# Kernel optimization log

Measured on AMD Instinct MI355X. Metric: run time of the kernel, lower is better.

Reference implementation:

```python
import jax, jax.numpy as jnp
import numpy as np

C_LOGIT = 10.0  # logit clipping constant C from __init__
NEG_INF = -1e8


def setup_inputs() -> dict:
    key = jax.random.key(0)
    ks = jax.random.split(key, 10)
    B, S, E, H = 512, 256, 128, 128
    u = lambda k, sh: jax.random.uniform(k, sh, jnp.float32, -0.1, 0.1)
    return {
        "low_context_vector": jax.random.normal(ks[0], (B, S, E), jnp.float32),
        "original_node": jax.random.uniform(ks[1], (S, 2), jnp.float32),
        "mask": jnp.zeros((B, S), jnp.float32),
        # learned parameters
        "low_init_w": jax.random.uniform(ks[2], (2 * E,), jnp.float32, -1.0, 1.0),
        "Wc": u(ks[3], (E, E)),   "bc": u(ks[4], (E,)),     # low_h_context_embed
        "Wv": u(ks[5], (2 * E, E)), "bv": u(ks[6], (E,)),   # low_v_weight_embed
        "Wq": u(ks[7], (E, H)),                              # pointer query proj
        "Wref": u(ks[8], (E, H)),                            # pointer ref proj
        "v": u(ks[9], (H,)),                                 # pointer score vector
    }


def _decode(cv, mask, low_init_w, Wc, bc, Wv, bv, Wq, Wref, v, key):
    B, S, E = cv.shape
    h_bar = jnp.mean(cv, axis=1) @ Wc + bc              # [B,E]
    rest0 = low_init_w @ Wv + bv                        # [E]
    query0 = h_bar + rest0[None, :]                     # [B,E]
    ref = cv @ Wref                                     # [B,S,H], hoisted out of loop
    mask = mask.at[:, 0].set(1.0)                       # start node visited
    keys = jax.random.split(key, S - 1)
    binds = jnp.arange(B)

    def step(carry, k):
        mask, query, init_h, i = carry
        u_ = jnp.tanh((query @ Wq)[:, None, :] + ref) @ v      # [B,S]
        logits = jnp.where(mask > 0, NEG_INF, C_LOGIT * jnp.tanh(u_))
        logp = jax.nn.log_softmax(logits, axis=-1)
        g = jax.random.gumbel(k, logits.shape, logits.dtype)
        idx = jnp.argmax(logits + g, axis=-1)                  # Categorical sample, [B]
        lp = jnp.take_along_axis(logp, idx[:, None], axis=1)[:, 0]
        mask = mask.at[binds, idx].set(1.0)
        h = cv[binds, idx]                                     # gathered embedding [B,E]
        init_h = jnp.where(i == 0, h, init_h)                  # first pick cached
        query = h_bar + (jnp.concatenate([init_h, h], axis=-1) @ Wv + bv)
        return (mask, query, init_h, i + 1), (idx, lp)

    init = (mask, query0, jnp.zeros((B, E), cv.dtype), jnp.int32(0))
    _, (idxs, lps) = jax.lax.scan(step, init, keys)
    return idxs.T, lps.T  # [B, S-1] each


def reference(low_context_vector, original_node, mask, low_init_w, Wc, bc, Wv, bv, Wq, Wref, v):
    # original_node only feeds a printed local_reward in the torch code; it does
    # not affect the returned (indices, log_probs), so it is unused here.
    return _decode(low_context_vector, mask, low_init_w, Wc, bc, Wv, bv, Wq, Wref, v,
                   jax.random.key(42))
```

## Files before the change

### kernel.cpp

```cpp
#include <hip/hip_runtime.h>
#include <hip/hip_bf16.h>
#include <stdint.h>
#include <math.h>

#define NBATCH 512
#define NS 256
#define NE 128
#define NH 128
#define NSTEPS 255
#define NEGINF -1e8f
#define SENT_NEG -1e30f

__device__ __forceinline__ uint32_t rotl32(uint32_t x, uint32_t r) {
  return (x << r) | (x >> (32u - r));
}

__device__ __forceinline__ void tf2x32(uint32_t k0, uint32_t k1,
                                       uint32_t x0, uint32_t x1,
                                       uint32_t& o0, uint32_t& o1) {
  uint32_t ks2 = k0 ^ k1 ^ 0x1BD11BDAu;
  x0 += k0; x1 += k1;
#define TF_R4(a,b,c,d) \
  x0 += x1; x1 = rotl32(x1,a); x1 ^= x0; \
  x0 += x1; x1 = rotl32(x1,b); x1 ^= x0; \
  x0 += x1; x1 = rotl32(x1,c); x1 ^= x0; \
  x0 += x1; x1 = rotl32(x1,d); x1 ^= x0;
  TF_R4(13,15,26,6)   x0 += k1;  x1 += ks2 + 1u;
  TF_R4(17,29,16,24)  x0 += ks2; x1 += k0 + 2u;
  TF_R4(13,15,26,6)   x0 += k0;  x1 += k1 + 3u;
  TF_R4(17,29,16,24)  x0 += k1;  x1 += ks2 + 4u;
  TF_R4(13,15,26,6)   x0 += ks2; x1 += k0 + 5u;
#undef TF_R4
  o0 = x0; o1 = x1;
}

__device__ __forceinline__ float gumbel_of(uint2 key, uint32_t j) {
  uint32_t o0, o1;
  tf2x32(key.x, key.y, 0u, j, o0, o1);
  uint32_t bits = o0 ^ o1;
  float f = __uint_as_float((bits >> 9) | 0x3f800000u) - 1.0f;
  float u = (f == 0.0f) ? 1.17549435e-38f : f;
  float l1 = -logf(u);
  return -logf(l1);
}

__device__ __forceinline__ float nr_tanh(float x) {
  const float Chi = 2.8853900432586670f;
  const float Clo = 3.8519259822379735e-08f;
  float m = fmaf(x, Chi, x * Clo);
  m = fminf(m, 126.0f);
  float tt = __builtin_amdgcn_exp2f(m);
  float d  = tt + 1.0f;
  float r  = __builtin_amdgcn_rcpf(d);
  r = r * fmaf(-d, r, 2.0f);
  return fmaf(-2.0f, r, 1.0f);
}

__device__ __forceinline__ double dot32(const float4* __restrict__ a,
                                        const float4* __restrict__ bp) {
  double s = 0.0;
#pragma unroll
  for (int q = 0; q < 8; ++q) {
    float4 x = a[q], y = bp[q];
    s += (double)x.x * (double)y.x + (double)x.y * (double)y.y
       + (double)x.z * (double)y.z + (double)x.w * (double)y.w;
  }
  return s;
}

__device__ __forceinline__ double dot4d(float4 a, float4 b) {
  return ((double)a.x * (double)b.x + (double)a.y * (double)b.y)
       + ((double)a.z * (double)b.z + (double)a.w * (double)b.w);
}

__global__ void k1_mats(const float* __restrict__ Wv, const float* __restrict__ Wq,
                        const float* __restrict__ liw, const float* __restrict__ bvv,
                        float* __restrict__ M1T, float* __restrict__ M2T,
                        float* __restrict__ rest0) {
  int e = blockIdx.x, h = threadIdx.x;
  __shared__ float wrow[NE];
  if (e < 256) {
    wrow[h] = Wv[e * NE + h];
    __syncthreads();
    double a = 0.0;
    for (int k = 0; k < NE; ++k) a += (double)wrow[k] * (double)Wq[k * NH + h];
    if (e < 128) M1T[h * NE + e] = (float)a;
    else         M2T[h * NE + (e - 128)] = (float)a;
  } else {
    double a = 0.0;
    for (int k = 0; k < 2 * NE; ++k) a += (double)liw[k] * (double)Wv[k * NE + h];
    rest0[h] = (float)a + bvv[h];
  }
}

__global__ void k2_base(const float* __restrict__ cv, const float* __restrict__ Wc,
                        const float* __restrict__ bc, const float* __restrict__ bvv,
                        const float* __restrict__ Wq, const float* __restrict__ rest0,
                        double* __restrict__ qqbase, float* __restrict__ qq0) {
  int b = blockIdx.x, h = threadIdx.x;
  int b256 = b << 8;
  __shared__ float meanL[NE], hbarL[NE];
  double ms = 0.0;
  for (int s = 0; s < NS; ++s) ms += (double)cv[((size_t)b256 + s) * NE + h];
  meanL[h] = (float)(ms * (1.0 / 256.0));
  __syncthreads();
  double a = 0.0;
  for (int e = 0; e < NE; ++e) a += (double)meanL[e] * (double)Wc[e * NE + h];
  hbarL[h] = (float)a + bc[h];
  __syncthreads();
  double ab = 0.0, a0 = 0.0;
  for (int k = 0; k < NE; ++k) {
    double w = (double)Wq[k * NH + h];
    ab += (double)(hbarL[k] + bvv[k]) * w;
    a0 += (double)(hbarL[k] + rest0[k]) * w;
  }
  qqbase[(size_t)b * NH + h] = ab;
  qq0[(size_t)b * NH + h] = (float)a0;
}

__global__ __launch_bounds__(256)
void k_a2v2(const float* __restrict__ cv, const float* __restrict__ M2T,
            double* __restrict__ A2) {
  const int b  = blockIdx.x >> 3;
  const int s0 = (blockIdx.x & 7) << 5;
  const int t  = threadIdx.x;
  const int sl = t >> 7;
  const int h  = t & 127;
  const int b256 = b << 8;
  __shared__ float cvS[32][129];
  for (int idx = t; idx < 32 * NE; idx += 256) {
    int r = idx >> 7, c = idx & 127;
    cvS[r][c] = cv[((size_t)(b256 + s0 + r)) * NE + c];
  }
  __syncthreads();
  float4 m2r[32];
  {
    const float4* m2p = (const float4*)(M2T + (size_t)h * NE);
#pragma unroll
    for (int q = 0; q < 32; ++q) m2r[q] = m2p[q];
  }
#pragma unroll 1
  for (int it = 0; it < 16; ++it) {
    const int sLoc = (it << 1) + sl;
    const float4* cr4 = (const float4*)&cvS[sLoc][0];
    double c0 = 0, c1 = 0, c2 = 0, c3 = 0;
#pragma unroll
    for (int q = 0; q < 8; ++q) {
      c0 += dot4d(cr4[q * 4 + 0], m2r[q * 4 + 0]);
      c1 += dot4d(cr4[q * 4 + 1], m2r[q * 4 + 1]);
      c2 += dot4d(cr4[q * 4 + 2], m2r[q * 4 + 2]);
      c3 += dot4d(cr4[q * 4 + 3], m2r[q * 4 + 3]);
    }
    A2[((size_t)(b256 + s0 + sLoc)) * NH + h] = (c0 + c1) + (c2 + c3);
  }
}

struct MainSh {
  alignas(16) float  qq[NH];
  alignas(16) float  vvf[NH];
  alignas(8)  double partA[NS];
  float  logitArr[NS];
  alignas(8)  double base128[NH];
  uint2  keyL[NSTEPS];
  float  redV[8];
  float  redS[8];
  int    redI[8];
};

struct PreSh {
  float cvS[NS][33];
  float wS[32][NH];
};

template <int MODE>
__global__ __launch_bounds__(512, 4)
void decode_main(const float* __restrict__ cv,
                 const float* __restrict__ mask_in,
                 const float* __restrict__ Wref,
                 const float* __restrict__ vvec,
                 const double* __restrict__ qqbase,
                 const float* __restrict__ M1T,
                 const float* __restrict__ M2T,
                 const float* __restrict__ qq0,
                 const double* __restrict__ A2,
                 float* __restrict__ out) {
  const int b = blockIdx.x;
  const int t = threadIdx.x;
  const int b256 = b << 8;
  const int i = t & 255;
  const int halfo = t >> 8;
  const int hb = halfo << 6;

  __shared__ union { PreSh pre; MainSh m; } sh;
  __shared__ short rowIdA[NS], rowIdB[NS], posA[NS], posB[NS];
  __shared__ int nActSh[2], jSh[2], tmp8[4];
  __shared__ alignas(16) float refScratch[NE];

  bool act0 = false;
  if (t < NS) {
    act0 = !((t == 0) || (mask_in[(size_t)b256 + t] > 0.0f));
    uint64_t mb = __ballot(act0);
    int lane = t & 63, w = t >> 6;
    int pre = __popcll(mb & (((uint64_t)1 << lane) - 1));
    if (lane == 0) tmp8[w] = (int)__popcll(mb);
    posA[t] = (short)pre;
  }
  __syncthreads();
  if (t < NS) {
    int base = 0;
    for (int k = 0; k < (t >> 6); ++k) base += tmp8[k];
    int p = base + (int)posA[t];
    if (act0) rowIdA[p] = (short)t;
    posA[t] = (short)p;
  }
  if (t == 0) {
    nActSh[0] = tmp8[0] + tmp8[1] + tmp8[2] + tmp8[3];
    jSh[0] = -1;
  }
  __syncthreads();
  const int nAct0 = nActSh[0];

  const int myRow0 = (i < nAct0) ? (int)rowIdA[i] : 0;
  float refr[64];
#pragma unroll
  for (int j = 0; j < 64; ++j) refr[j] = 0.0f;

  for (int ec = 0; ec < 4; ++ec) {
    __syncthreads();
    for (int ii = t; ii < 32 * NH; ii += 512) {
      int r = ii >> 7, c = ii & 127;
      sh.pre.wS[r][c] = Wref[(ec * 32 + r) * NH + c];
    }
    for (int ii = t; ii < NS * 32; ii += 512) {
      int r = ii >> 5, c = ii & 31;
      sh.pre.cvS[r][c] = cv[((size_t)b256 + r) * NE + ec * 32 + c];
    }
    __syncthreads();
    for (int hc = 0; hc < 8; ++hc) {
      double a[8] = {0,0,0,0,0,0,0,0};
      for (int e = 0; e < 32; ++e) {
        double cd = (double)sh.pre.cvS[myRow0][e];
        const float* wp = &sh.pre.wS[e][hb + hc * 8];
#pragma unroll
        for (int j = 0; j < 8; ++j) a[j] += cd * (double)wp[j];
      }
#pragma unroll
      for (int j = 0; j < 8; ++j) refr[hc * 8 + j] += (float)a[j];
    }
  }
  __syncthreads();

  if (t < NSTEPS) {
    uint32_t o0, o1;
    tf2x32(0u, 42u, 0u, (uint32_t)t, o0, o1);
    sh.m.keyL[t] = make_uint2(o0, o1);
  }
  if (t < NH) {
    sh.m.vvf[t] = vvec[t];
    sh.m.qq[t] = qq0[(size_t)b * NH + t];
  }
  __syncthreads();

  float g = 0.0f;
  if (halfo && i < nAct0)
    g = gumbel_of(sh.m.keyL[0], (uint32_t)(b256 + myRow0));

  for (int step = 0; step < NSTEPS; ++step) {
    const int cur = step & 1;
    const short* rowId_c = cur ? rowIdB : rowIdA;
    const short* pos_c   = cur ? posB   : posA;
    short* rowId_n = cur ? rowIdA : rowIdB;
    short* pos_n   = cur ? posA   : posB;
    const int nA    = nActSh[cur];
    const int jPrev = jSh[cur];
    const bool active = (i < nA);
    const int myRow = active ? (int)rowId_c[i] : 0;

    if (jPrev >= 0 && i == jPrev) {
      const float4* rs4 = (const float4*)(refScratch + hb);
#pragma unroll
      for (int q = 0; q < 16; ++q) {
        float4 v4 = rs4[q];
        refr[4 * q + 0] = v4.x; refr[4 * q + 1] = v4.y;
        refr[4 * q + 2] = v4.z; refr[4 * q + 3] = v4.w;
      }
    }

    double accH = 0.0;
    if (active) {
      double a0 = 0, a1 = 0, a2 = 0, a3 = 0;
      const float4* qq4 = (const float4*)(sh.m.qq + hb);
      const float4* vv4 = (const float4*)(sh.m.vvf + hb);
#pragma unroll
      for (int q = 0; q < 16; ++q) {
        float4 qv = qq4[q];
        float4 wv = vv4[q];
        a0 += (double)nr_tanh(qv.x + refr[4 * q + 0]) * (double)wv.x;
        a1 += (double)nr_tanh(qv.y + refr[4 * q + 1]) * (double)wv.y;
        a2 += (double)nr_tanh(qv.z + refr[4 * q + 2]) * (double)wv.z;
        a3 += (double)nr_tanh(qv.w + refr[4 * q + 3]) * (double)wv.w;
      }
      accH = (a0 + a1) + (a2 + a3);
      if (!halfo) sh.m.partA[i] = accH;
    }
    __syncthreads();

    if (halfo) {
      float val = SENT_NEG; int vRow = 0x7fffffff; float term = 0.0f;
      if (active) {
        float u_ = (float)(sh.m.partA[i] + accH);
        float logit = 10.0f * (float)tanh((double)u_);
        sh.m.logitArr[myRow] = logit;
        term = expf(logit);
        val = logit + g;
        vRow = myRow;
      }
      float bvv = val; int bR = vRow; float bss = term;
#pragma unroll
      for (int mm = 1; mm <= 32; mm <<= 1) {
        float ov = __shfl_xor(bvv, mm, 64);
        int   oR = __shfl_xor(bR,  mm, 64);
        float os = __shfl_xor(bss, mm, 64);
        bss += os;
        if (ov > bvv || (ov == bvv && oR < bR)) { bvv = ov; bR = oR; }
      }
      if ((t & 63) == 0) {
        int w = t >> 6;
        sh.m.redV[w] = bvv; sh.m.redI[w] = bR; sh.m.redS[w] = bss;
      }
    }
    __syncthreads();

    float BV = sh.m.redV[4]; int BR = sh.m.redI[4];
#pragma unroll
    for (int k = 5; k < 8; ++k) {
      float ov = sh.m.redV[k]; int oR = sh.m.redI[k];
      if (ov > BV || (ov == BV && oR < BR)) { BV = ov; BR = oR; }
    }
    if ((unsigned)BR > 255u) BR = 0;
    const int BI = BR;
    const int jj = (int)pos_c[BI];

    double a2v = 0.0;
    if (MODE == 1 && step > 0 && step + 1 < NSTEPS && t < NH)
      a2v = A2[(size_t)(b256 + BI) * NH + t];

    if (t == 0) {
      float SS = (sh.m.redS[4] + sh.m.redS[5]) + (sh.m.redS[6] + sh.m.redS[7]);
      float lp = sh.m.logitArr[BI] - (float)log((double)SS);
      out[(size_t)b * NSTEPS + step] = (float)BI;
      out[(size_t)NBATCH * NSTEPS + (size_t)b * NSTEPS + step] = lp;
      nActSh[cur ^ 1] = nA - 1;
      jSh[cur ^ 1] = (jj < nA - 1) ? jj : -1;
    }

    if (t < NS) {
      int donorRow = (int)rowId_c[nA - 1];
      short rid = (t == jj) ? (short)donorRow : rowId_c[t];
      rowId_n[t] = rid;
      if (t < nA - 1) pos_n[rid] = (short)t;
    }
    if (jj < nA - 1 && i == nA - 1) {
      float4* rs4 = (float4*)(refScratch + hb);
#pragma unroll
      for (int q = 0; q < 16; ++q)
        rs4[q] = make_float4(refr[4 * q + 0], refr[4 * q + 1],
                             refr[4 * q + 2], refr[4 * q + 3]);
    }

    if (halfo && step + 1 < NSTEPS) {
      int nA_next = nA - 1;
      if (i < nA_next) {
        int ridN = (i == jj) ? (int)rowId_c[nA - 1] : myRow;
        g = gumbel_of(sh.m.keyL[step + 1], (uint32_t)(b256 + ridN));
      }
    }

    if (step + 1 < NSTEPS) {
      if (MODE == 1) {
        if (step == 0) {
          const int hq = t >> 2, kq = t & 3;
          const float4* hrow = (const float4*)(cv + (size_t)(b256 + BI) * NE + kq * 32);
          const float4* m1p  = (const float4*)(M1T + (size_t)hq * NE + kq * 32);
          double am = dot32(hrow, m1p);
          am += __shfl_xor(am, 1, 64);
          am += __shfl_xor(am, 2, 64);
          if (kq == 0) {
            double dbase = qqbase[(size_t)b * NH + hq] + am;
            sh.m.base128[hq] = dbase;
            sh.m.qq[hq] = (float)(dbase + A2[(size_t)(b256 + BI) * NH + hq]);
          }
        } else if (t < NH) {
          sh.m.qq[t] = (float)(sh.m.base128[t] + a2v);
        }
      } else {
        const int hq = t >> 2, kq = t & 3;
        const float4* hrow = (const float4*)(cv + (size_t)(b256 + BI) * NE + kq * 32);
        const float4* m2p  = (const float4*)(M2T + (size_t)hq * NE + kq * 32);
        double a2 = dot32(hrow, m2p);
        a2 += __shfl_xor(a2, 1, 64);
        a2 += __shfl_xor(a2, 2, 64);
        if (step == 0) {
          const float4* m1p = (const float4*)(M1T + (size_t)hq * NE + kq * 32);
          double am = dot32(hrow, m1p);
          am += __shfl_xor(am, 1, 64);
          am += __shfl_xor(am, 2, 64);
          if (kq == 0) {
            double dbase = qqbase[(size_t)b * NH + hq] + am;
            sh.m.base128[hq] = dbase;
            sh.m.qq[hq] = (float)(dbase + a2);
          }
        } else if (kq == 0) {
          sh.m.qq[hq] = (float)(sh.m.base128[hq] + a2);
        }
      }
    }
    __syncthreads();
  }
}

__device__ __forceinline__ float fast_tanh_ref(float x) {
  const float Chi = 2.8853900432586670f;
  const float Clo = 3.8519259822379735e-08f;
  float m = fmaf(x, Chi, x * Clo);
  float tt = exp2f(m);
  return 1.0f - 2.0f / (tt + 1.0f);
}

struct MainShR {
  float  query[NE];
  float  qq[NH];
  float  hbar[NE];
  float  inith[NE];
  float  hcur[NE];
  alignas(16) double vvd[NH];
  float  logitArr[NS];
  float  maskArr[NS];
  uint2  keyL[NSTEPS];
  float  meanv[NE];
  float  redV[4];
  int    redI[4];
  double redS[4];
  int    idxSh;
};
struct PreShR {
  float cvS[NS][33];
  float wS[32][NH];
};

__global__ __launch_bounds__(256, 2)
void decoder_kernel_ref(const float* __restrict__ cv, const float* __restrict__ mask_in,
                        const float* __restrict__ liw, const float* __restrict__ Wc,
                        const float* __restrict__ bc, const float* __restrict__ Wv,
                        const float* __restrict__ bv, const float* __restrict__ Wq,
                        const float* __restrict__ Wref, const float* __restrict__ vvec,
                        float* __restrict__ out) {
  const int b = blockIdx.x;
  const int t = threadIdx.x;
  const int b256 = b << 8;
  __shared__ union { PreShR pre; MainShR m; } sh;

  float refr[NH];
#pragma unroll
  for (int h = 0; h < NH; ++h) refr[h] = 0.0f;
  for (int ec = 0; ec < 4; ++ec) {
    const int e0 = ec * 32;
    __syncthreads();
    for (int i = t; i < 32 * NH; i += 256) {
      int r = i >> 7, h = i & 127;
      sh.pre.wS[r][h] = Wref[(e0 + r) * NH + h];
    }
    for (int i = t; i < NS * 32; i += 256) {
      int s2 = i >> 5, j = i & 31;
      sh.pre.cvS[s2][j] = cv[((size_t)b256 + s2) * NE + e0 + j];
    }
    __syncthreads();
#pragma unroll
    for (int hc = 0; hc < 16; ++hc) {
      double a[8] = {0,0,0,0,0,0,0,0};
      for (int e = 0; e < 32; ++e) {
        double cd = (double)sh.pre.cvS[t][e];
#pragma unroll
        for (int j = 0; j < 8; ++j) a[j] += cd * (double)sh.pre.wS[e][hc * 8 + j];
      }
#pragma unroll
      for (int j = 0; j < 8; ++j) refr[hc * 8 + j] += (float)a[j];
    }
  }
  __syncthreads();

  if (t < NSTEPS) {
    uint32_t o0, o1;
    tf2x32(0u, 42u, 0u, (uint32_t)t, o0, o1);
    sh.m.keyL[t] = make_uint2(o0, o1);
  }
  if (t < NH) sh.m.vvd[t] = (double)vvec[t];
  sh.m.maskArr[t] = (mask_in[(size_t)b256 + t] > 0.0f || t == 0) ? 1.0f : 0.0f;
  if (t < NE) {
    double s64 = 0.0;
    for (int s2 = 0; s2 < NS; ++s2) s64 += (double)cv[((size_t)b256 + s2) * NE + t];
    sh.m.meanv[t] = (float)(s64 * (1.0 / 256.0));
  }
  __syncthreads();
  if (t < NE) {
    double acc = 0.0;
    for (int e = 0; e < NE; ++e) acc += (double)sh.m.meanv[e] * (double)Wc[e * NE + t];
    float hbv = (float)acc + bc[t];
    sh.m.hbar[t] = hbv;
    double acc2 = 0.0;
    for (int k = 0; k < 2 * NE; ++k) acc2 += (double)liw[k] * (double)Wv[k * NE + t];
    float r0 = (float)acc2 + bv[t];
    sh.m.query[t] = hbv + r0;
  }
  __syncthreads();

  for (int step = 0; step < NSTEPS; ++step) {
    if (t < NH) {
      double acc = 0.0;
      for (int k = 0; k < NE; ++k) acc += (double)sh.m.query[k] * (double)Wq[k * NH + t];
      sh.m.qq[t] = (float)acc;
    }
    __syncthreads();

    float logit;
    bool masked = (sh.m.maskArr[t] != 0.0f);
    if (!masked) {
      double a0 = 0.0, a1 = 0.0, a2 = 0.0, a3 = 0.0;
      const float4*  qq4 = (const float4*)sh.m.qq;
      const double2* vv2 = (const double2*)sh.m.vvd;
#pragma unroll
      for (int h4 = 0; h4 < 32; ++h4) {
        float4  q  = qq4[h4];
        double2 va = vv2[2 * h4];
        double2 vb = vv2[2 * h4 + 1];
        a0 += (double)fast_tanh_ref(q.x + refr[4 * h4 + 0]) * va.x;
        a1 += (double)fast_tanh_ref(q.y + refr[4 * h4 + 1]) * va.y;
        a2 += (double)fast_tanh_ref(q.z + refr[4 * h4 + 2]) * vb.x;
        a3 += (double)fast_tanh_ref(q.w + refr[4 * h4 + 3]) * vb.y;
      }
      float u_ = (float)((a0 + a1) + (a2 + a3));
      logit = 10.0f * (float)tanh((double)u_);
    } else {
      logit = NEGINF;
    }
    sh.m.logitArr[t] = logit;

    uint2 key = sh.m.keyL[step];
    uint32_t j = (uint32_t)(b256 + t);
    uint32_t o0, o1;
    tf2x32(key.x, key.y, 0u, j, o0, o1);
    uint32_t bits = o0 ^ o1;
    float f = __uint_as_float((bits >> 9) | 0x3f800000u) - 1.0f;
    float u = (f == 0.0f) ? 1.17549435e-38f : f;
    float l1 = (float)(-log((double)u));
    float g  = (float)(-log((double)l1));
    float val = logit + g;
    double term = exp((double)logit);

    float bv_ = val; int bi = t; double bs = term;
#pragma unroll
    for (int m = 1; m <= 32; m <<= 1) {
      float  ov = __shfl_xor(bv_, m, 64);
      int    oi = __shfl_xor(bi,  m, 64);
      double os = __shfl_xor(bs,  m, 64);
      if (ov > bv_ || (ov == bv_ && oi < bi)) { bv_ = ov; bi = oi; }
      bs += os;
    }
    int w = t >> 6;
    if ((t & 63) == 0) { sh.m.redV[w] = bv_; sh.m.redI[w] = bi; sh.m.redS[w] = bs; }
    __syncthreads();

    if (t == 0) {
      float BV = sh.m.redV[0]; int BI = sh.m.redI[0];
      for (int k = 1; k < 4; ++k) {
        float ov = sh.m.redV[k]; int oi = sh.m.redI[k];
        if (ov > BV || (ov == BV && oi < BI)) { BV = ov; BI = oi; }
      }
      double SS = ((sh.m.redS[0] + sh.m.redS[1]) + (sh.m.redS[2] + sh.m.redS[3]));
      sh.m.idxSh = BI;
      float lp = sh.m.logitArr[BI] - (float)log(SS);
      out[(size_t)b * NSTEPS + step] = (float)BI;
      out[(size_t)NBATCH * NSTEPS + (size_t)b * NSTEPS + step] = lp;
    }
    __syncthreads();

    int idx = sh.m.idxSh;
    if (t == idx) sh.m.maskArr[t] = 1.0f;
    if (t < NE) {
      float hc = cv[((size_t)b256 + idx) * NE + t];
      sh.m.hcur[t] = hc;
      if (step == 0) sh.m.inith[t] = hc;
    }
    __syncthreads();

    if (t < NE) {
      double acc2 = 0.0;
      for (int k = 0; k < NE; ++k) acc2 += (double)sh.m.inith[k] * (double)Wv[k * NE + t];
      for (int k = 0; k < NE; ++k) acc2 += (double)sh.m.hcur[k] * (double)Wv[(NE + k) * NE + t];
      float mm = (float)acc2 + bv[t];
      sh.m.query[t] = sh.m.hbar[t] + mm;
    }
    __syncthreads();
  }
}

extern "C" void kernel_launch(void* const* d_in, const int* in_sizes, int n_in,
                              void* d_out, int out_size, void* d_ws, size_t ws_size,
                              hipStream_t stream) {
  const float* cv   = (const float*)d_in[0];
  const float* mask = (const float*)d_in[2];
  const float* liw  = (const float*)d_in[3];
  const float* Wc   = (const float*)d_in[4];
  const float* bc   = (const float*)d_in[5];
  const float* Wv   = (const float*)d_in[6];
  const float* bv   = (const float*)d_in[7];
  const float* Wq   = (const float*)d_in[8];
  const float* Wref = (const float*)d_in[9];
  const float* vv   = (const float*)d_in[10];
  (void)in_sizes; (void)n_in; (void)out_size;

  const size_t SZ_QQB = (size_t)NBATCH * NH * sizeof(double);
  const size_t SZ_M   = (size_t)NE * NH * sizeof(float);
  const size_t SZ_QQ0 = (size_t)NBATCH * NH * sizeof(float);
  const size_t SZ_A2  = (size_t)NBATCH * NS * NH * sizeof(double);
  const size_t need_min = SZ_QQB + 2 * SZ_M + SZ_QQ0 + 512;
  const size_t need_pre = need_min + SZ_A2;

  if (ws_size >= need_min) {
    char* p = (char*)d_ws;
    double* qqbase = (double*)p;            p += SZ_QQB;
    float*  M1T    = (float*)p;             p += SZ_M;
    float*  M2T    = (float*)p;             p += SZ_M;
    float*  qq0    = (float*)p;             p += SZ_QQ0;
    float*  rest0  = (float*)p;             p += 512;
    double* A2     = (double*)p;

    k1_mats<<<257, 128, 0, stream>>>(Wv, Wq, liw, bv, M1T, M2T, rest0);
    k2_base<<<NBATCH, 128, 0, stream>>>(cv, Wc, bc, bv, Wq, rest0, qqbase, qq0);
    if (ws_size >= need_pre) {
      k_a2v2<<<NBATCH * 8, 256, 0, stream>>>(cv, M2T, A2);
      decode_main<1><<<NBATCH, 512, 0, stream>>>(cv, mask, Wref, vv, qqbase, M1T,
                                                 M2T, qq0, A2, (float*)d_out);
    } else {
      decode_main<0><<<NBATCH, 512, 0, stream>>>(cv, mask, Wref, vv, qqbase, M1T,
                                                 M2T, qq0, nullptr, (float*)d_out);
    }
  } else {
    decoder_kernel_ref<<<NBATCH, 256, 0, stream>>>(cv, mask, liw, Wc, bc, Wv, bv,
                                                   Wq, Wref, vv, (float*)d_out);
  }
}
```

Baseline: 3.588 ms.

## Split A2 precompute dot products across lane pairs and rotate decode wave-to-row mapping

The A2 precompute kernel now has each pair of threads split the 128-wide dot product into two halves, combining them with a lane shuffle. This halves the per-thread register array and adds an occupancy hint. The shared row stride is padded to 132 so float4 reads stay aligned. Separately, the decode kernel rotates which 64-row chunk each wavefront handles based on the block index, likely to spread memory access patterns across blocks. This risks extra shuffle overhead and changes which thread owns which row, which could affect any code that assumes i==t&255.

```diff
diff --git a/kernel.cpp b/kernel.cpp
--- a/kernel.cpp
+++ b/kernel.cpp
@@ -118,40 +118,40 @@
   qq0[(size_t)b * NH + h] = (float)a0;
 }
 
-__global__ __launch_bounds__(256)
-void k_a2v2(const float* __restrict__ cv, const float* __restrict__ M2T,
+__global__ __launch_bounds__(256, 4)
+void k_a2v3(const float* __restrict__ cv, const float* __restrict__ M2T,
             double* __restrict__ A2) {
   const int b  = blockIdx.x >> 3;
   const int s0 = (blockIdx.x & 7) << 5;
   const int t  = threadIdx.x;
-  const int sl = t >> 7;
-  const int h  = t & 127;
+  const int h  = t >> 1;
+  const int kh = t & 1;
   const int b256 = b << 8;
-  __shared__ float cvS[32][129];
+  __shared__ float cvS[32][132];
   for (int idx = t; idx < 32 * NE; idx += 256) {
     int r = idx >> 7, c = idx & 127;
     cvS[r][c] = cv[((size_t)(b256 + s0 + r)) * NE + c];
   }
   __syncthreads();
-  float4 m2r[32];
+  float4 m2r[16];
   {
-    const float4* m2p = (const float4*)(M2T + (size_t)h * NE);
-#pragma unroll
-    for (int q = 0; q < 32; ++q) m2r[q] = m2p[q];
-  }
-#pragma unroll 1
-  for (int it = 0; it < 16; ++it) {
-    const int sLoc = (it << 1) + sl;
-    const float4* cr4 = (const float4*)&cvS[sLoc][0];
-    double c0 = 0, c1 = 0, c2 = 0, c3 = 0;
-#pragma unroll
-    for (int q = 0; q < 8; ++q) {
-      c0 += dot4d(cr4[q * 4 + 0], m2r[q * 4 + 0]);
-      c1 += dot4d(cr4[q * 4 + 1], m2r[q * 4 + 1]);
-      c2 += dot4d(cr4[q * 4 + 2], m2r[q * 4 + 2]);
-      c3 += dot4d(cr4[q * 4 + 3], m2r[q * 4 + 3]);
-    }
-    A2[((size_t)(b256 + s0 + sLoc)) * NH + h] = (c0 + c1) + (c2 + c3);
+    const float4* m2p = (const float4*)(M2T + (size_t)h * NE + kh * 64);
+#pragma unroll
+    for (int q = 0; q < 16; ++q) m2r[q] = m2p[q];
+  }
+#pragma unroll 2
+  for (int sLoc = 0; sLoc < 32; ++sLoc) {
+    const float4* cr4 = ((const float4*)&cvS[sLoc][0]) + kh * 16;
+    double c0 = 0.0, c1 = 0.0;
+#pragma unroll
+    for (int q = 0; q < 16; q += 2) {
+      c0 += dot4d(cr4[q],     m2r[q]);
+      c1 += dot4d(cr4[q + 1], m2r[q + 1]);
+    }
+    double s = c0 + c1;
+    s += __shfl_xor(s, 1, 64);
+    if (kh == 0)
+      A2[((size_t)(b256 + s0 + sLoc)) * NH + h] = s;
   }
 }
 
@@ -187,7 +187,8 @@
   const int b = blockIdx.x;
   const int t = threadIdx.x;
   const int b256 = b << 8;
-  const int i = t & 255;
+  const int chunk = (((t >> 6) & 3) + b) & 3;
+  const int i = (chunk << 6) | (t & 63);
   const int halfo = t >> 8;
   const int hb = halfo << 6;
 
@@ -638,7 +639,7 @@
     k1_mats<<<257, 128, 0, stream>>>(Wv, Wq, liw, bv, M1T, M2T, rest0);
     k2_base<<<NBATCH, 128, 0, stream>>>(cv, Wc, bc, bv, Wq, rest0, qqbase, qq0);
     if (ws_size >= need_pre) {
-      k_a2v2<<<NBATCH * 8, 256, 0, stream>>>(cv, M2T, A2);
+      k_a2v3<<<NBATCH * 8, 256, 0, stream>>>(cv, M2T, A2);
       decode_main<1><<<NBATCH, 512, 0, stream>>>(cv, mask, Wref, vv, qqbase, M1T,
                                                  M2T, qq0, A2, (float*)d_out);
     } else {
```

New measurement: 3.163 ms. 1.13x faster.
